# Performance work log

Hardware: AMD Instinct MI355X
Metric: run time of the kernel (lower is better)

The kernel has to match this reference:

```python
import jax, jax.numpy as jnp
import numpy as np

D_HEAD = 64
D_MODEL = 1024
N_HEADS = D_MODEL // D_HEAD
MAX_TOKENS = 2048


def setup_inputs() -> dict:
    key = jax.random.key(0)
    ks = jax.random.split(key, 5)
    batch, pos = 2, 2048
    # kaiming_normal_ on (n_heads, d_model, d_head): fan_in = d_model*d_head -> std = sqrt(2/fan_in)
    std_qkv = np.sqrt(2.0 / (D_MODEL * D_HEAD)).astype(np.float32)
    # xavier_normal_ on (d_model, d_model): std = sqrt(2/(fan_in+fan_out))
    std_out = np.sqrt(2.0 / (D_MODEL + D_MODEL)).astype(np.float32)
    return {
        "residual_stream": jax.random.normal(ks[0], (batch, pos, D_MODEL), dtype=jnp.float32),
        "weight_query": jax.random.normal(ks[1], (N_HEADS, D_MODEL, D_HEAD), dtype=jnp.float32) * std_qkv,
        "weight_key": jax.random.normal(ks[2], (N_HEADS, D_MODEL, D_HEAD), dtype=jnp.float32) * std_qkv,
        "weight_value": jax.random.normal(ks[3], (N_HEADS, D_MODEL, D_HEAD), dtype=jnp.float32) * std_qkv,
        "weight_out": jax.random.normal(ks[4], (D_MODEL, D_MODEL), dtype=jnp.float32) * std_out,
    }


def reference(residual_stream, weight_query, weight_key, weight_value, weight_out):
    # QKV projections: [b, p, m] x [h, m, d] -> [b, h, p, d]
    q = jnp.einsum('bpm,hmd->bhpd', residual_stream, weight_query)
    k = jnp.einsum('bpm,hmd->bhpd', residual_stream, weight_key)
    v = jnp.einsum('bpm,hmd->bhpd', residual_stream, weight_value)

    n_tokens = residual_stream.shape[1]
    # scaled scores [b, h, dest, src]
    scores = jnp.einsum('bhqd,bhkd->bhqk', q, k) / jnp.sqrt(jnp.float32(D_HEAD))
    # causal mask: -inf above the diagonal
    causal = jnp.tril(jnp.ones((n_tokens, n_tokens), dtype=bool))
    scores = jnp.where(causal, scores, jnp.float32(-jnp.inf))
    pattern = jax.nn.softmax(scores, axis=-1)

    attn = jnp.einsum('bhqk,bhkd->bhqd', pattern, v)  # [b, h, dest, d_head]
    # concat heads -> [b, p, h*d_head]
    b, h, p, d = attn.shape
    attn_concat = jnp.transpose(attn, (0, 2, 1, 3)).reshape(b, p, h * d)
    return jnp.einsum('bpm,mn->bpn', attn_concat, weight_out)
```

## Files before the change

### kernel.cpp

```cpp
#include <hip/hip_runtime.h>
#include <hip/hip_bf16.h>
#include <stdint.h>


typedef __bf16 bf16x8 __attribute__((ext_vector_type(8)));
typedef float f32x4 __attribute__((ext_vector_type(4)));
typedef float f32x16 __attribute__((ext_vector_type(16)));
typedef unsigned short u16;

__device__ __forceinline__ u16 f2bf(float f) {
  unsigned u = __float_as_uint(f);
  u += 0x7fffu + ((u >> 16) & 1u);
  return (u16)(u >> 16);
}

__device__ __forceinline__ uint32_t cvtpk(float lo, float hi) {
  uint32_t r;
  asm("v_cvt_pk_bf16_f32 %0, %1, %2" : "=v"(r) : "v"(lo), "v"(hi));
  return r;
}

__device__ __forceinline__ void pl32swap(uint32_t& a, uint32_t& b) {
  asm volatile("v_permlane32_swap_b32 %0, %1" : "+v"(a), "+v"(b));
}

__global__ __launch_bounds__(256) void xcvt_k(const float* __restrict__ in,
                                              u16* __restrict__ out) {
  int i = (blockIdx.x * 256 + threadIdx.x) * 8;
  float4 f0 = *reinterpret_cast<const float4*>(in + i);
  float4 f1 = *reinterpret_cast<const float4*>(in + i + 4);
  u16 tmp[8] = {f2bf(f0.x), f2bf(f0.y), f2bf(f0.z), f2bf(f0.w),
                f2bf(f1.x), f2bf(f1.y), f2bf(f1.z), f2bf(f1.w)};
  *reinterpret_cast<uint4*>(out + i) = *reinterpret_cast<uint4*>(tmp);
}

__global__ __launch_bounds__(256) void transpose_cvt_k(const float* __restrict__ in,
                                                       u16* __restrict__ out,
                                                       int R, int C) {
  __shared__ u16 tile[64][80];
  int b = blockIdx.z;
  int r0 = blockIdx.x * 64, c0 = blockIdx.y * 64;
  const float* ip = in + (size_t)b * R * C;
  u16* op = out + (size_t)b * R * C;
  int t = threadIdx.x;
  int r = t >> 2, cb = (t & 3) * 16;
  const float4* src = reinterpret_cast<const float4*>(ip + (size_t)(r0 + r) * C + c0 + cb);
  u16 tmp[16];
#pragma unroll
  for (int v = 0; v < 4; v++) {
    float4 f = src[v];
    tmp[v * 4 + 0] = f2bf(f.x);
    tmp[v * 4 + 1] = f2bf(f.y);
    tmp[v * 4 + 2] = f2bf(f.z);
    tmp[v * 4 + 3] = f2bf(f.w);
  }
  *reinterpret_cast<uint4*>(&tile[r][cb]) = *reinterpret_cast<uint4*>(&tmp[0]);
  *reinterpret_cast<uint4*>(&tile[r][cb + 8]) = *reinterpret_cast<uint4*>(&tmp[8]);
  __syncthreads();
  int c = t >> 2, rb = (t & 3) * 16;
  uint4 outv[2];
  u16* tp = reinterpret_cast<u16*>(outv);
#pragma unroll
  for (int j = 0; j < 16; j++) tp[j] = tile[rb + j][c];
  uint4* dst = reinterpret_cast<uint4*>(op + (size_t)(c0 + c) * R + r0 + rb);
  dst[0] = outv[0];
  dst[1] = outv[1];
}

__global__ __launch_bounds__(256) void transpose_qkv_k(const float* __restrict__ Wq,
                                                       const float* __restrict__ Wk,
                                                       const float* __restrict__ Wv,
                                                       u16* __restrict__ outBase) {
  __shared__ u16 tile[64][80];
  int z = blockIdx.z;
  int sel = z >> 4, head = z & 15;
  const float* W = (sel == 0) ? Wq : (sel == 1 ? Wk : Wv);
  const float* ip = W + (size_t)head * 65536;
  u16* op = outBase + (size_t)sel * 1048576 + (size_t)head * 65536;
  int r0 = blockIdx.x * 64;
  int t = threadIdx.x;
  int r = t >> 2, cb = (t & 3) * 16;
  const float4* src = reinterpret_cast<const float4*>(ip + (size_t)(r0 + r) * 64 + cb);
  u16 tmp[16];
#pragma unroll
  for (int v = 0; v < 4; v++) {
    float4 f = src[v];
    tmp[v * 4 + 0] = f2bf(f.x);
    tmp[v * 4 + 1] = f2bf(f.y);
    tmp[v * 4 + 2] = f2bf(f.z);
    tmp[v * 4 + 3] = f2bf(f.w);
  }
  *reinterpret_cast<uint4*>(&tile[r][cb]) = *reinterpret_cast<uint4*>(&tmp[0]);
  *reinterpret_cast<uint4*>(&tile[r][cb + 8]) = *reinterpret_cast<uint4*>(&tmp[8]);
  __syncthreads();
  int c = t >> 2, rb = (t & 3) * 16;
  uint4 outv[2];
  u16* tp = reinterpret_cast<u16*>(outv);
#pragma unroll
  for (int j = 0; j < 16; j++) tp[j] = tile[rb + j][c];
  uint4* dst = reinterpret_cast<uint4*>(op + (size_t)c * 1024 + r0 + rb);
  dst[0] = outv[0];
  dst[1] = outv[1];
}

__device__ __forceinline__ void gload16(const u16* g, u16* l) {
  __builtin_amdgcn_global_load_lds(
      (__attribute__((address_space(1))) void*)(g),
      (__attribute__((address_space(3))) void*)(l), 16, 0, 0);
}

__device__ __forceinline__ void gemm128_core(const u16* __restrict__ A,
                                             const u16* __restrict__ BT,
                                             int m0, int n0,
                                             f32x4 (&acc)[4][4]) {
  __shared__ __align__(16) u16 As[2][128][64];
  __shared__ __align__(16) u16 Bs[2][128][64];
  int t = threadIdx.x, l = t & 63;
  int w = t >> 6, wm = w & 1, wn = w >> 1;
  int l15 = l & 15, q4 = l >> 4;
  int r8 = l >> 3;
  int cs = ((l & 7) ^ r8) * 8;
  int swz = l15 & 7;
  int srow = w * 32 + r8;
  const u16* ga = A + (size_t)(m0 + srow) * 1024 + cs;
  const u16* gb = BT + (size_t)(n0 + srow) * 1024 + cs;
  f32x4 z4 = {0.f, 0.f, 0.f, 0.f};
#pragma unroll
  for (int mi = 0; mi < 4; mi++)
#pragma unroll
    for (int nt = 0; nt < 4; nt++) acc[mi][nt] = z4;

#pragma unroll
  for (int i = 0; i < 4; i++) {
    gload16(ga + (size_t)(i * 8) * 1024, &As[0][w * 32 + i * 8][0]);
    gload16(gb + (size_t)(i * 8) * 1024, &Bs[0][w * 32 + i * 8][0]);
  }
  __syncthreads();

  for (int step = 0; step < 16; step++) {
    int cur = step & 1;
    if (step < 15) {
      int k0 = (step + 1) * 64;
#pragma unroll
      for (int i = 0; i < 4; i++) {
        gload16(ga + (size_t)(i * 8) * 1024 + k0, &As[cur ^ 1][w * 32 + i * 8][0]);
        gload16(gb + (size_t)(i * 8) * 1024 + k0, &Bs[cur ^ 1][w * 32 + i * 8][0]);
      }
    }
#pragma unroll
    for (int kk = 0; kk < 2; kk++) {
      bf16x8 af[4], bfr[4];
#pragma unroll
      for (int mi = 0; mi < 4; mi++)
        af[mi] = *reinterpret_cast<const bf16x8*>(
            &As[cur][wm * 64 + mi * 16 + l15][((kk * 4 + q4) ^ swz) * 8]);
#pragma unroll
      for (int nt = 0; nt < 4; nt++)
        bfr[nt] = *reinterpret_cast<const bf16x8*>(
            &Bs[cur][wn * 64 + nt * 16 + l15][((kk * 4 + q4) ^ swz) * 8]);
#pragma unroll
      for (int mi = 0; mi < 4; mi++)
#pragma unroll
        for (int nt = 0; nt < 4; nt++)
          acc[mi][nt] = __builtin_amdgcn_mfma_f32_16x16x32_bf16(af[mi], bfr[nt], acc[mi][nt], 0, 0, 0);
    }
    __syncthreads();
  }
}

__global__ __launch_bounds__(256) void qkv_gemm128_k(const u16* __restrict__ A,
                                                     const u16* __restrict__ BT,
                                                     u16* __restrict__ Q,
                                                     u16* __restrict__ K,
                                                     u16* __restrict__ VT2) {
  const float QSCALE = 0.125f * 1.44269504088896340736f;
  int m0 = blockIdx.x * 128, n0 = blockIdx.y * 128;
  f32x4 acc[4][4];
  gemm128_core(A, BT, m0, n0, acc);
  int t = threadIdx.x, l = t & 63;
  int w = t >> 6, wm = w & 1, wn = w >> 1;
  int l15 = l & 15, q4 = l >> 4;
#pragma unroll
  for (int mi = 0; mi < 4; mi++) {
#pragma unroll
    for (int nt = 0; nt < 4; nt++) {
#pragma unroll
      for (int r = 0; r < 4; r++) {
        int m = m0 + wm * 64 + mi * 16 + q4 * 4 + r;
        int n = n0 + wn * 64 + nt * 16 + l15;
        int wsel = n >> 10, h = (n >> 6) & 15, d = n & 63;
        int b = m >> 11, p = m & 2047;
        size_t bh = (size_t)(b * 16 + h);
        float v = acc[mi][nt][r];
        if (wsel == 0)
          Q[(bh * 2048 + p) * 64 + d] = f2bf(v * QSCALE);
        else if (wsel == 1)
          K[(bh * 2048 + p) * 64 + d] = f2bf(v);
        else
          VT2[((bh * 32 + (p >> 6)) * 64 + d) * 64 + (p & 63)] = f2bf(v);
      }
    }
  }
}

__global__ __launch_bounds__(256) void out_gemm128_k(const u16* __restrict__ A,
                                                     const u16* __restrict__ BT,
                                                     float* __restrict__ O) {
  int m0 = blockIdx.x * 128, n0 = blockIdx.y * 128;
  f32x4 acc[4][4];
  gemm128_core(A, BT, m0, n0, acc);
  int t = threadIdx.x, l = t & 63;
  int w = t >> 6, wm = w & 1, wn = w >> 1;
  int l15 = l & 15, q4 = l >> 4;
#pragma unroll
  for (int mi = 0; mi < 4; mi++) {
#pragma unroll
    for (int nt = 0; nt < 4; nt++) {
#pragma unroll
      for (int r = 0; r < 4; r++) {
        int m = m0 + wm * 64 + mi * 16 + q4 * 4 + r;
        int n = n0 + wn * 64 + nt * 16 + l15;
        O[(size_t)m * 1024 + n] = acc[mi][nt][r];
      }
    }
  }
}

__global__ __launch_bounds__(256) void attn_k(const u16* __restrict__ Q,
                                              const u16* __restrict__ K,
                                              const u16* __restrict__ VT2,
                                              u16* __restrict__ A) {
  __shared__ __align__(16) u16 Ks[2][64][64];
  __shared__ __align__(16) u16 Vs[2][64][64];
  __shared__ float rsbuf[4][32];
  int pr = blockIdx.x, h = blockIdx.y, b = blockIdx.z;
  int qt = b ? (15 - pr) : pr;
  size_t bh = (size_t)(b * 16 + h);
  const u16* Qp = Q + bh * 2048 * 64;
  const u16* Kp = K + bh * 2048 * 64;
  const u16* Vt = VT2 + bh * 32 * 64 * 64;
  int t = threadIdx.x, l = t & 63, w = t >> 6;
  int l31 = l & 31, hi = l >> 5;
  int r8 = l >> 3, cs = ((l & 7) ^ r8) * 8;
  int swz = l31 & 7;
  const float NEG = -1e30f;
  int nkt = 2 * qt + 2;
  const u16* kbase = Kp + (size_t)(w * 16 + r8) * 64 + cs;
  const u16* vbase = Vt + (size_t)(w * 16 + r8) * 64 + cs;
  int qrow = qt * 128 + w * 32 + l31;

  bf16x8 qb[4];
#pragma unroll
  for (int kc = 0; kc < 4; kc++)
    qb[kc] = *reinterpret_cast<const bf16x8*>(Qp + (size_t)qrow * 64 + kc * 16 + hi * 8);

  f32x16 accO[2];
#pragma unroll
  for (int dh = 0; dh < 2; dh++)
#pragma unroll
    for (int r = 0; r < 16; r++) accO[dh][r] = 0.f;
  float rs = 0.f;

#pragma unroll
  for (int j = 0; j < 2; j++) {
    gload16(kbase + (size_t)(j * 512), &Ks[0][w * 16 + j * 8][0]);
    gload16(vbase + (size_t)(j * 512), &Vs[0][w * 16 + j * 8][0]);
  }
  __syncthreads();

  for (int kt = 0; kt < nkt; kt++) {
    int cur = kt & 1;
    if (kt < nkt - 1) {
      size_t off = (size_t)(kt + 1) * 4096;
#pragma unroll
      for (int j = 0; j < 2; j++) {
        gload16(kbase + off + j * 512, &Ks[cur ^ 1][w * 16 + j * 8][0]);
        gload16(vbase + off + j * 512, &Vs[cur ^ 1][w * 16 + j * 8][0]);
      }
    }

    f32x16 st[2];
#pragma unroll
    for (int kvh = 0; kvh < 2; kvh++)
#pragma unroll
      for (int r = 0; r < 16; r++) st[kvh][r] = 0.f;
    __builtin_amdgcn_s_setprio(1);
#pragma unroll
    for (int kc = 0; kc < 4; kc++) {
      bf16x8 ka0 = *reinterpret_cast<const bf16x8*>(
          &Ks[cur][l31][((2 * kc + hi) ^ swz) * 8]);
      bf16x8 ka1 = *reinterpret_cast<const bf16x8*>(
          &Ks[cur][32 + l31][((2 * kc + hi) ^ swz) * 8]);
      st[0] = __builtin_amdgcn_mfma_f32_32x32x16_bf16(ka0, qb[kc], st[0], 0, 0, 0);
      st[1] = __builtin_amdgcn_mfma_f32_32x32x16_bf16(ka1, qb[kc], st[1], 0, 0, 0);
    }
    __builtin_amdgcn_s_setprio(0);

    if (kt >= 2 * qt) {
      int kvb = kt * 64;
#pragma unroll
      for (int kvh = 0; kvh < 2; kvh++)
#pragma unroll
        for (int r = 0; r < 16; r++) {
          int kv = kvb + kvh * 32 + (r & 3) + 8 * (r >> 2) + 4 * hi;
          if (kv > qrow) st[kvh][r] = NEG;
        }
    }

#pragma unroll
    for (int kvh = 0; kvh < 2; kvh++)
#pragma unroll
      for (int r = 0; r < 16; r++) {
        float p = exp2f(st[kvh][r]);
        st[kvh][r] = p;
        rs += p;
      }

    bf16x8 pa[4];
#pragma unroll
    for (int ks = 0; ks < 4; ks++) {
      const f32x16& pp = st[ks >> 1];
      const int s8 = (ks & 1) * 8;
      uint32_t x0 = cvtpk(pp[s8 + 0], pp[s8 + 1]);
      uint32_t x1 = cvtpk(pp[s8 + 2], pp[s8 + 3]);
      uint32_t y0 = cvtpk(pp[s8 + 4], pp[s8 + 5]);
      uint32_t y1 = cvtpk(pp[s8 + 6], pp[s8 + 7]);
      pl32swap(x0, y0);
      pl32swap(x1, y1);
      uint32_t wds[4] = {x0, x1, y0, y1};
      pa[ks] = *reinterpret_cast<const bf16x8*>(wds);
    }

    __builtin_amdgcn_s_setprio(1);
#pragma unroll
    for (int dh = 0; dh < 2; dh++)
#pragma unroll
      for (int ks = 0; ks < 4; ks++) {
        bf16x8 vb = *reinterpret_cast<const bf16x8*>(
            &Vs[cur][dh * 32 + l31][((2 * ks + hi) ^ swz) * 8]);
        accO[dh] = __builtin_amdgcn_mfma_f32_32x32x16_bf16(pa[ks], vb, accO[dh], 0, 0, 0);
      }
    __builtin_amdgcn_s_setprio(0);
    __syncthreads();
  }

  rs += __shfl_xor(rs, 32, 64);
  if (hi == 0) rsbuf[w][l31] = rs;
  __syncthreads();
#pragma unroll
  for (int r = 0; r < 16; r++) {
    int ql = (r & 3) + 8 * (r >> 2) + 4 * hi;
    float inv = 1.f / rsbuf[w][ql];
    int prow = qt * 128 + w * 32 + ql;
    size_t base = ((size_t)(b * 2048 + prow)) * 1024 + h * 64;
    A[base + l31] = f2bf(accO[0][r] * inv);
    A[base + 32 + l31] = f2bf(accO[1][r] * inv);
  }
}

extern "C" void kernel_launch(void* const* d_in, const int* in_sizes, int n_in,
                              void* d_out, int out_size, void* d_ws, size_t ws_size,
                              hipStream_t stream) {
  const float* X  = (const float*)d_in[0];
  const float* Wq = (const float*)d_in[1];
  const float* Wk = (const float*)d_in[2];
  const float* Wv = (const float*)d_in[3];
  const float* Wo = (const float*)d_in[4];
  float* out = (float*)d_out;

  u16* ws = (u16*)d_ws;
  u16* WqT = ws;
  u16* WoT = WqT + 3145728;
  u16* Xb  = WoT + 1048576;
  u16* Qb  = Xb + 4194304;
  u16* Kb  = Qb + 4194304;
  u16* VT2 = Kb + 4194304;
  u16* Ab  = Xb;

  xcvt_k<<<dim3(2048), 256, 0, stream>>>(X, Xb);
  transpose_qkv_k<<<dim3(16, 1, 48), 256, 0, stream>>>(Wq, Wk, Wv, WqT);
  transpose_cvt_k<<<dim3(16, 16, 1), 256, 0, stream>>>(Wo, WoT, 1024, 1024);

  qkv_gemm128_k<<<dim3(32, 24), 256, 0, stream>>>(Xb, WqT, Qb, Kb, VT2);
  attn_k<<<dim3(16, 16, 2), 256, 0, stream>>>(Qb, Kb, VT2, Ab);
  out_gemm128_k<<<dim3(32, 8), 256, 0, stream>>>(Ab, WoT, out);
}
```

Measured before the change: 217.2 us.

## Replace QKV GEMM with 256x256 tile, 8-wave kernel and phased async staging

The QKV projection GEMM moves from 128x128 tiles with 4 waves to 256x256 tiles with 8 waves, staged through 128KB of double-buffered dynamic shared memory. Each K-step is split into four phases that interleave global-to-LDS loads of the next tile with MFMA work, using explicit vmcnt waits, barriers and setprio. The larger tile raises arithmetic intensity and data reuse per block. In exchange the grid shrinks to 192 blocks at one block per CU, which on 256 CUs leaves some CUs idle, and the hand-scheduled waitcnt pipeline is delicate to get right.

```diff
diff --git a/kernel.cpp b/kernel.cpp
--- a/kernel.cpp
+++ b/kernel.cpp
@@ -168,25 +168,117 @@
   }
 }
 
-__global__ __launch_bounds__(256) void qkv_gemm128_k(const u16* __restrict__ A,
-                                                     const u16* __restrict__ BT,
-                                                     u16* __restrict__ Q,
-                                                     u16* __restrict__ K,
-                                                     u16* __restrict__ VT2) {
+__global__ __launch_bounds__(512, 1) void qkv_gemm256_k(const u16* __restrict__ A,
+                                                        const u16* __restrict__ BT,
+                                                        u16* __restrict__ Q,
+                                                        u16* __restrict__ K,
+                                                        u16* __restrict__ VT2) {
+  extern __shared__ __align__(16) u16 sm[];
+  u16* As = sm;
+  u16* Bs = sm + 2 * 256 * 64;
   const float QSCALE = 0.125f * 1.44269504088896340736f;
-  int m0 = blockIdx.x * 128, n0 = blockIdx.y * 128;
-  f32x4 acc[4][4];
-  gemm128_core(A, BT, m0, n0, acc);
-  int t = threadIdx.x, l = t & 63;
-  int w = t >> 6, wm = w & 1, wn = w >> 1;
+  int m0 = blockIdx.x * 256, n0 = blockIdx.y * 256;
+  int t = threadIdx.x, l = t & 63, w = t >> 6;
+  int wm = w >> 2, wn = w & 3;
   int l15 = l & 15, q4 = l >> 4;
-#pragma unroll
-  for (int mi = 0; mi < 4; mi++) {
+  int r8 = l >> 3;
+  int cs = ((l & 7) ^ r8) * 8;
+  int swz = l15 & 7;
+  const u16* gA = A + (size_t)m0 * 1024 + cs;
+  const u16* gB = BT + (size_t)n0 * 1024 + cs;
+
+  f32x4 acc[8][4];
+  f32x4 z4 = {0.f, 0.f, 0.f, 0.f};
+#pragma unroll
+  for (int mi = 0; mi < 8; mi++)
+#pragma unroll
+    for (int nt = 0; nt < 4; nt++) acc[mi][nt] = z4;
+
+  auto stageB = [&](int buf, int h, int kcol) {
+#pragma unroll
+    for (int j = 0; j < 2; j++) {
+      int row = 128 * h + w * 16 + j * 8;
+      gload16(gB + (size_t)(row + r8) * 1024 + kcol,
+              &Bs[((size_t)buf * 256 + row) * 64]);
+    }
+  };
+  auto stageA2 = [&](int buf, int qsel, int kcol) {
+#pragma unroll
+    for (int j = 0; j < 2; j++) {
+      int qq = qsel + 2 * j;
+      int row = 64 * qq + w * 8;
+      gload16(gA + (size_t)(row + r8) * 1024 + kcol,
+              &As[((size_t)buf * 256 + row) * 64]);
+    }
+  };
+
+  stageB(0, 0, 0);
+  stageB(0, 1, 0);
+  stageA2(0, 0, 0);
+  stageA2(0, 1, 0);
+
+  for (int T = 0; T < 16; T++) {
+    int buf = T & 1, nbuf = buf ^ 1;
+    int nk = (T + 1) * 64;
+    bool more = T < 15;
+    bf16x8 bfr[4][2];
+#pragma unroll
+    for (int p = 0; p < 4; p++) {
+      if (p == 0) {
+        asm volatile("s_waitcnt vmcnt(2)" ::: "memory");
+      } else if (p == 2) {
+        if (more)
+          asm volatile("s_waitcnt vmcnt(4)" ::: "memory");
+        else
+          asm volatile("s_waitcnt vmcnt(0)" ::: "memory");
+      }
+      __builtin_amdgcn_s_barrier();
+      if (more) {
+        if (p == 0) stageB(nbuf, 0, nk);
+        else if (p == 1) stageB(nbuf, 1, nk);
+        else if (p == 2) stageA2(nbuf, 0, nk);
+        else stageA2(nbuf, 1, nk);
+      }
+      if (p == 0) {
+#pragma unroll
+        for (int nt = 0; nt < 4; nt++) {
+          int row = wn * 64 + nt * 16 + l15;
+#pragma unroll
+          for (int kk = 0; kk < 2; kk++)
+            bfr[nt][kk] = *reinterpret_cast<const bf16x8*>(
+                &Bs[((size_t)buf * 256 + row) * 64 + ((kk * 4 + q4) ^ swz) * 8]);
+        }
+      }
+      bf16x8 af[2][2];
+#pragma unroll
+      for (int j = 0; j < 2; j++) {
+        int mi = 2 * p + j;
+        int row = wm * 128 + mi * 16 + l15;
+#pragma unroll
+        for (int kk = 0; kk < 2; kk++)
+          af[j][kk] = *reinterpret_cast<const bf16x8*>(
+              &As[((size_t)buf * 256 + row) * 64 + ((kk * 4 + q4) ^ swz) * 8]);
+      }
+      __builtin_amdgcn_s_setprio(1);
+#pragma unroll
+      for (int kk = 0; kk < 2; kk++)
+#pragma unroll
+        for (int j = 0; j < 2; j++)
+#pragma unroll
+          for (int nt = 0; nt < 4; nt++)
+            acc[2 * p + j][nt] = __builtin_amdgcn_mfma_f32_16x16x32_bf16(
+                af[j][kk], bfr[nt][kk], acc[2 * p + j][nt], 0, 0, 0);
+      __builtin_amdgcn_s_setprio(0);
+    }
+  }
+
+#pragma unroll
+  for (int mi = 0; mi < 8; mi++) {
 #pragma unroll
     for (int nt = 0; nt < 4; nt++) {
 #pragma unroll
       for (int r = 0; r < 4; r++) {
-        int m = m0 + wm * 64 + mi * 16 + q4 * 4 + r;
+        int m = m0 + wm * 128 + mi * 16 + q4 * 4 + r;
         int n = n0 + wn * 64 + nt * 16 + l15;
         int wsel = n >> 10, h = (n >> 6) & 15, d = n & 63;
         int b = m >> 11, p = m & 2047;
@@ -381,7 +473,7 @@
   transpose_qkv_k<<<dim3(16, 1, 48), 256, 0, stream>>>(Wq, Wk, Wv, WqT);
   transpose_cvt_k<<<dim3(16, 16, 1), 256, 0, stream>>>(Wo, WoT, 1024, 1024);
 
-  qkv_gemm128_k<<<dim3(32, 24), 256, 0, stream>>>(Xb, WqT, Qb, Kb, VT2);
+  qkv_gemm256_k<<<dim3(16, 12), 512, 131072, stream>>>(Xb, WqT, Qb, Kb, VT2);
   attn_k<<<dim3(16, 16, 2), 256, 0, stream>>>(Qb, Kb, VT2, Ab);
   out_gemm128_k<<<dim3(32, 8), 256, 0, stream>>>(Ab, WoT, out);
 }
```

New measurement: 216.7 us. No clear change (-0.2%).

## Replace QKV GEMM with 256x256 tile, 512-thread, 4-stage async-load pipeline

Applied to the files above, without the earlier changes.

The QKV projection GEMM moves from a 128x128 tile with 256 threads to a 256x256 tile with 512 threads. It uses 128KB of dynamic LDS holding a 4-deep ring of K=32 slices, filled by direct global-to-LDS loads issued three stages ahead. Fine-grained vmcnt waits replace full syncs, and s_setprio raises priority around the MFMA block. The goal is more data reuse per tile and better overlap of memory loads with MFMA work. The trade-off is fewer blocks (192) on a GPU with 256 CUs, which leaves some CUs idle, plus a heavy LDS footprint that limits the kernel to one block per CU.

```diff
diff --git a/kernel.cpp b/kernel.cpp
--- a/kernel.cpp
+++ b/kernel.cpp
@@ -168,25 +168,87 @@
   }
 }
 
-__global__ __launch_bounds__(256) void qkv_gemm128_k(const u16* __restrict__ A,
-                                                     const u16* __restrict__ BT,
-                                                     u16* __restrict__ Q,
-                                                     u16* __restrict__ K,
-                                                     u16* __restrict__ VT2) {
+__global__ __launch_bounds__(512, 1) void qkv_gemm256_k(const u16* __restrict__ A,
+                                                        const u16* __restrict__ BT,
+                                                        u16* __restrict__ Q,
+                                                        u16* __restrict__ K,
+                                                        u16* __restrict__ VT2) {
+  extern __shared__ __align__(16) u16 sm[];
+  u16* As = sm;
+  u16* Bs = sm + 4 * 256 * 32;
   const float QSCALE = 0.125f * 1.44269504088896340736f;
-  int m0 = blockIdx.x * 128, n0 = blockIdx.y * 128;
-  f32x4 acc[4][4];
-  gemm128_core(A, BT, m0, n0, acc);
-  int t = threadIdx.x, l = t & 63;
-  int w = t >> 6, wm = w & 1, wn = w >> 1;
+  int m0 = blockIdx.x * 256, n0 = blockIdx.y * 256;
+  int t = threadIdx.x, l = t & 63, w = t >> 6;
+  int wm = w >> 2, wn = w & 3;
   int l15 = l & 15, q4 = l >> 4;
-#pragma unroll
-  for (int mi = 0; mi < 4; mi++) {
+  int key = (l15 & 3) ^ ((l15 >> 2) & 3);
+  int rl = l >> 2;
+  int cg = (l & 3) ^ (rl & 3) ^ ((rl >> 2) & 3);
+  size_t lsrc = (size_t)rl * 1024 + cg * 8;
+  const u16* gA = A + (size_t)m0 * 1024;
+  const u16* gB = BT + (size_t)n0 * 1024;
+  int arow0 = w * 32;
+
+  f32x4 acc[8][4];
+  f32x4 z4 = {0.f, 0.f, 0.f, 0.f};
+#pragma unroll
+  for (int mi = 0; mi < 8; mi++)
+#pragma unroll
+    for (int nt = 0; nt < 4; nt++) acc[mi][nt] = z4;
+
+  auto stage = [&](int buf, int k0) {
+    u16* ab = As + (size_t)buf * 8192;
+    u16* bb = Bs + (size_t)buf * 8192;
+    gload16(gA + (size_t)arow0 * 1024 + k0 + lsrc, ab + (size_t)arow0 * 32);
+    gload16(gA + (size_t)(arow0 + 16) * 1024 + k0 + lsrc, ab + (size_t)(arow0 + 16) * 32);
+    gload16(gB + (size_t)arow0 * 1024 + k0 + lsrc, bb + (size_t)arow0 * 32);
+    gload16(gB + (size_t)(arow0 + 16) * 1024 + k0 + lsrc, bb + (size_t)(arow0 + 16) * 32);
+  };
+
+  stage(0, 0);
+  stage(1, 32);
+  stage(2, 64);
+
+  for (int s = 0; s < 32; s++) {
+    int buf = s & 3;
+    if (s < 30)
+      asm volatile("s_waitcnt vmcnt(8)" ::: "memory");
+    else if (s == 30)
+      asm volatile("s_waitcnt vmcnt(4)" ::: "memory");
+    else
+      asm volatile("s_waitcnt vmcnt(0)" ::: "memory");
+    __builtin_amdgcn_s_barrier();
+
+    const u16* ab = As + (size_t)buf * 8192;
+    const u16* bb = Bs + (size_t)buf * 8192;
+    bf16x8 af[8], bfr[4];
+#pragma unroll
+    for (int mi = 0; mi < 8; mi++)
+      af[mi] = *reinterpret_cast<const bf16x8*>(
+          &ab[(size_t)(wm * 128 + mi * 16 + l15) * 32 + (size_t)((q4 ^ key) * 8)]);
+#pragma unroll
+    for (int nt = 0; nt < 4; nt++)
+      bfr[nt] = *reinterpret_cast<const bf16x8*>(
+          &bb[(size_t)(wn * 64 + nt * 16 + l15) * 32 + (size_t)((q4 ^ key) * 8)]);
+
+    if (s + 3 < 32) stage((s + 3) & 3, (s + 3) * 32);
+
+    __builtin_amdgcn_s_setprio(1);
+#pragma unroll
+    for (int mi = 0; mi < 8; mi++)
+#pragma unroll
+      for (int nt = 0; nt < 4; nt++)
+        acc[mi][nt] = __builtin_amdgcn_mfma_f32_16x16x32_bf16(af[mi], bfr[nt], acc[mi][nt], 0, 0, 0);
+    __builtin_amdgcn_s_setprio(0);
+  }
+
+#pragma unroll
+  for (int mi = 0; mi < 8; mi++) {
 #pragma unroll
     for (int nt = 0; nt < 4; nt++) {
 #pragma unroll
       for (int r = 0; r < 4; r++) {
-        int m = m0 + wm * 64 + mi * 16 + q4 * 4 + r;
+        int m = m0 + wm * 128 + mi * 16 + q4 * 4 + r;
         int n = n0 + wn * 64 + nt * 16 + l15;
         int wsel = n >> 10, h = (n >> 6) & 15, d = n & 63;
         int b = m >> 11, p = m & 2047;
@@ -381,7 +443,7 @@
   transpose_qkv_k<<<dim3(16, 1, 48), 256, 0, stream>>>(Wq, Wk, Wv, WqT);
   transpose_cvt_k<<<dim3(16, 16, 1), 256, 0, stream>>>(Wo, WoT, 1024, 1024);
 
-  qkv_gemm128_k<<<dim3(32, 24), 256, 0, stream>>>(Xb, WqT, Qb, Kb, VT2);
+  qkv_gemm256_k<<<dim3(16, 12), 512, 131072, stream>>>(Xb, WqT, Qb, Kb, VT2);
   attn_k<<<dim3(16, 16, 2), 256, 0, stream>>>(Qb, Kb, VT2, Ab);
   out_gemm128_k<<<dim3(32, 8), 256, 0, stream>>>(Ab, WoT, out);
 }
```

Result: no change. 220.7 us (+1.6%).
